# Optimization experiments

Measured on AMD Instinct MI355X. Metric: run time of the kernel, lower is better.

The kernel has to match this reference:

```python
import jax, jax.numpy as jnp
import numpy as np


def setup_inputs() -> dict:
    key = jax.random.key(0)
    z = jax.random.normal(key, (8, 4096, 1024), dtype=jnp.float32)
    return {"z": z}


def reference(z):
    d = z.shape[-1]
    # sort descending along last dim
    z_sorted = -jnp.sort(-z, axis=-1)
    z_cumsum = jnp.cumsum(z_sorted, axis=-1)
    k = jnp.arange(1, d + 1, dtype=z.dtype)  # [d]
    rhs = 1 + k * z_sorted
    is_gt = (rhs > z_cumsum).astype(z.dtype)
    # largest k satisfying the support condition
    k_z = jnp.max(is_gt * k, axis=-1, keepdims=True)  # [..., 1]
    idx = k_z.astype(jnp.int32) - 1
    z_cumsum_k = jnp.take_along_axis(z_cumsum, idx, axis=-1)
    tau = (z_cumsum_k - 1) / k_z
    p = jnp.clip(z - tau, 0.0, None)
    return p
```

## Files before the change

kernel.cpp:

```cpp
#include <hip/hip_runtime.h>


#define ROW_D 1024
#define NEG_PAD -3.0e38f

typedef float f4 __attribute__((ext_vector_type(4)));

template <int CTRL, int RMASK>
__device__ __forceinline__ float dpp_mv(float x) {
    return __builtin_bit_cast(float, __builtin_amdgcn_update_dpp(
        __builtin_bit_cast(int, x), __builtin_bit_cast(int, x),
        CTRL, RMASK, 0xf, false));
}
__device__ __forceinline__ float dpp_sum_to63(float x) {
    x += dpp_mv<0x111, 0xf>(x);
    x += dpp_mv<0x112, 0xf>(x);
    x += dpp_mv<0x114, 0xf>(x);
    x += dpp_mv<0x118, 0xf>(x);
    x += dpp_mv<0x142, 0xa>(x);
    x += dpp_mv<0x143, 0xc>(x);
    return x;
}
__device__ __forceinline__ float dpp_max_to63(float x) {
    x = fmaxf(x, dpp_mv<0x111, 0xf>(x));
    x = fmaxf(x, dpp_mv<0x112, 0xf>(x));
    x = fmaxf(x, dpp_mv<0x114, 0xf>(x));
    x = fmaxf(x, dpp_mv<0x118, 0xf>(x));
    x = fmaxf(x, dpp_mv<0x142, 0xa>(x));
    x = fmaxf(x, dpp_mv<0x143, 0xc>(x));
    return x;
}
__device__ __forceinline__ float bcast63(float x) {
    return __builtin_bit_cast(float,
        __builtin_amdgcn_readlane(__builtin_bit_cast(int, x), 63));
}

__global__ __launch_bounds__(256) void sparsemax_kernel(
    const float* __restrict__ z, float* __restrict__ out, int nrows) {
    const int lane = (int)(threadIdx.x & 63u);
    const int row  = (int)(blockIdx.x << 2) + (int)(threadIdx.x >> 6);
    if (row >= nrows) return;

    const f4* __restrict__ zin = reinterpret_cast<const f4*>(z + (size_t)row * ROW_D);
    f4* __restrict__ pout      = reinterpret_cast<f4*>(out + (size_t)row * ROW_D);

    f4 v[4];
#pragma unroll
    for (int j = 0; j < 4; ++j) v[j] = zin[lane + 64 * j];

    float mj[4];
#pragma unroll
    for (int j = 0; j < 4; ++j)
        mj[j] = fmaxf(fmaxf(v[j].x, v[j].y), fmaxf(v[j].z, v[j].w));
    float m = fmaxf(fmaxf(mj[0], mj[1]), fmaxf(mj[2], mj[3]));
    m = bcast63(dpp_max_to63(m));
    const float lo0 = m - 1.0f;

    float c0 = NEG_PAD, c1 = NEG_PAD, c2 = NEG_PAD;
    int cnt = 0;
#pragma unroll
    for (int j = 0; j < 4; ++j) {
        const float e[4] = {v[j].x, v[j].y, v[j].z, v[j].w};
#pragma unroll
        for (int c = 0; c < 4; ++c) {
            const bool g = e[c] > lo0;
            c2 = g ? c1 : c2;
            c1 = g ? c0 : c1;
            c0 = g ? e[c] : c0;
            cnt += g ? 1 : 0;
        }
    }

    float t = lo0;
    if (__ballot(cnt > 3) == 0ULL) {
#pragma unroll 1
        for (int it = 0; it < 16; ++it) {
            const float d0 = c0 - t, d1 = c1 - t, d2 = c2 - t;
            const float s = fmaxf(d0, 0.0f) + (fmaxf(d1, 0.0f) + fmaxf(d2, 0.0f));
            int n = __popcll(__ballot(d0 > 0.0f));
            n += __popcll(__ballot(d1 > 0.0f));
            n += __popcll(__ballot(d2 > 0.0f));
            const float S = bcast63(dpp_sum_to63(s));
            const float t2 = t + (S - 1.0f) / (float)n;
            if (t2 - t <= 1e-6f) { t = t2; break; }
            t = t2;
        }
    } else {
#pragma unroll 1
        for (int it = 0; it < 24; ++it) {
            float sj[4];
            int n = 0;
#pragma unroll
            for (int j = 0; j < 4; ++j) {
                const float d0 = v[j].x - t, d1 = v[j].y - t;
                const float d2 = v[j].z - t, d3 = v[j].w - t;
                sj[j] = (fmaxf(d0, 0.0f) + fmaxf(d1, 0.0f)) +
                        (fmaxf(d2, 0.0f) + fmaxf(d3, 0.0f));
                n += __popcll(__ballot(d0 > 0.0f));
                n += __popcll(__ballot(d1 > 0.0f));
                n += __popcll(__ballot(d2 > 0.0f));
                n += __popcll(__ballot(d3 > 0.0f));
            }
            const float S = bcast63(dpp_sum_to63((sj[0] + sj[1]) + (sj[2] + sj[3])));
            const float t2 = t + (S - 1.0f) / (float)n;
            if (t2 - t <= 1e-6f) { t = t2; break; }
            t = t2;
        }
    }

#pragma unroll
    for (int j = 0; j < 4; ++j) {
        f4 o;
        o.x = fmaxf(v[j].x - t, 0.0f);
        o.y = fmaxf(v[j].y - t, 0.0f);
        o.z = fmaxf(v[j].z - t, 0.0f);
        o.w = fmaxf(v[j].w - t, 0.0f);
        __builtin_nontemporal_store(o, pout + lane + 64 * j);
    }
}

extern "C" void kernel_launch(void* const* d_in, const int* in_sizes, int n_in,
                              void* d_out, int out_size, void* d_ws, size_t ws_size,
                              hipStream_t stream) {
    const float* z = (const float*)d_in[0];
    float* out = (float*)d_out;
    const int n = in_sizes[0];
    const int nrows = n / ROW_D;
    const int blocks = (nrows + 3) / 4;
    sparsemax_kernel<<<blocks, 256, 0, stream>>>(z, out, nrows);
}
```

Baseline: 229.4 us.

## Process four rows per wave with register double-buffered prefetch of next row

Each wavefront now handles several consecutive rows, loading the next row into registers while computing tau for the current one. This hides global-load latency behind the iterative threshold search and cuts the grid to a quarter of the blocks. In exchange it uses more registers, may lower occupancy, and leaves fewer blocks to spread across the CUs.

```diff
diff --git a/kernel.cpp b/kernel.cpp
--- a/kernel.cpp
+++ b/kernel.cpp
@@ -2,6 +2,7 @@
 
 
 #define ROW_D 1024
+#define RPW   4
 #define NEG_PAD -3.0e38f
 
 typedef float f4 __attribute__((ext_vector_type(4)));
@@ -35,19 +36,7 @@
         __builtin_amdgcn_readlane(__builtin_bit_cast(int, x), 63));
 }
 
-__global__ __launch_bounds__(256) void sparsemax_kernel(
-    const float* __restrict__ z, float* __restrict__ out, int nrows) {
-    const int lane = (int)(threadIdx.x & 63u);
-    const int row  = (int)(blockIdx.x << 2) + (int)(threadIdx.x >> 6);
-    if (row >= nrows) return;
-
-    const f4* __restrict__ zin = reinterpret_cast<const f4*>(z + (size_t)row * ROW_D);
-    f4* __restrict__ pout      = reinterpret_cast<f4*>(out + (size_t)row * ROW_D);
-
-    f4 v[4];
-#pragma unroll
-    for (int j = 0; j < 4; ++j) v[j] = zin[lane + 64 * j];
-
+__device__ __forceinline__ float row_tau(const f4* __restrict__ v) {
     float mj[4];
 #pragma unroll
     for (int j = 0; j < 4; ++j)
@@ -107,15 +96,48 @@
             t = t2;
         }
     }
+    return t;
+}
+
+__global__ __launch_bounds__(256) void sparsemax_kernel(
+    const float* __restrict__ z, float* __restrict__ out, int nrows) {
+    const int lane  = (int)(threadIdx.x & 63u);
+    const int wslot = (int)(threadIdx.x >> 6);
+    const int base  = ((int)(blockIdx.x << 2) + wslot) * RPW;
+    if (base >= nrows) return;
+
+    f4 nxt[4], cur[4];
+    {
+        const f4* zr = reinterpret_cast<const f4*>(z + (size_t)base * ROW_D);
+#pragma unroll
+        for (int j = 0; j < 4; ++j) nxt[j] = zr[lane + 64 * j];
+    }
 
 #pragma unroll
-    for (int j = 0; j < 4; ++j) {
-        f4 o;
-        o.x = fmaxf(v[j].x - t, 0.0f);
-        o.y = fmaxf(v[j].y - t, 0.0f);
-        o.z = fmaxf(v[j].z - t, 0.0f);
-        o.w = fmaxf(v[j].w - t, 0.0f);
-        __builtin_nontemporal_store(o, pout + lane + 64 * j);
+    for (int i = 0; i < RPW; ++i) {
+        const int row = (base + i < nrows) ? base + i : nrows - 1;
+#pragma unroll
+        for (int j = 0; j < 4; ++j) cur[j] = nxt[j];
+
+        if (i + 1 < RPW) {
+            const int nrow = (base + i + 1 < nrows) ? base + i + 1 : nrows - 1;
+            const f4* zn = reinterpret_cast<const f4*>(z + (size_t)nrow * ROW_D);
+#pragma unroll
+            for (int j = 0; j < 4; ++j) nxt[j] = zn[lane + 64 * j];
+        }
+
+        const float t = row_tau(cur);
+
+        f4* po = reinterpret_cast<f4*>(out + (size_t)row * ROW_D);
+#pragma unroll
+        for (int j = 0; j < 4; ++j) {
+            f4 o;
+            o.x = fmaxf(cur[j].x - t, 0.0f);
+            o.y = fmaxf(cur[j].y - t, 0.0f);
+            o.z = fmaxf(cur[j].z - t, 0.0f);
+            o.w = fmaxf(cur[j].w - t, 0.0f);
+            __builtin_nontemporal_store(o, po + lane + 64 * j);
+        }
     }
 }
 
@@ -126,6 +148,7 @@
     float* out = (float*)d_out;
     const int n = in_sizes[0];
     const int nrows = n / ROW_D;
-    const int blocks = (nrows + 3) / 4;
+    const int rows_per_block = 4 * RPW;
+    const int blocks = (nrows + rows_per_block - 1) / rows_per_block;
     sparsemax_kernel<<<blocks, 256, 0, stream>>>(z, out, nrows);
 }
```

New measurement: 237.0 us. 3.3% more time.

## Split sparsemax into separate tau-computation and apply kernels

Applied to the files above, without the earlier changes.

Splits the fused kernel into two launches. The first computes each row's threshold and writes it to workspace, and the second rereads the input and applies the clip. The intent is to let each stage have simpler register usage and access patterns. The cost is reading the 128MB input twice plus an extra kernel launch.

```diff
diff --git a/kernel.cpp b/kernel.cpp
--- a/kernel.cpp
+++ b/kernel.cpp
@@ -35,15 +35,13 @@
         __builtin_amdgcn_readlane(__builtin_bit_cast(int, x), 63));
 }
 
-__global__ __launch_bounds__(256) void sparsemax_kernel(
-    const float* __restrict__ z, float* __restrict__ out, int nrows) {
+__global__ __launch_bounds__(256) void tau_kernel(
+    const float* __restrict__ z, float* __restrict__ taus, int nrows) {
     const int lane = (int)(threadIdx.x & 63u);
     const int row  = (int)(blockIdx.x << 2) + (int)(threadIdx.x >> 6);
     if (row >= nrows) return;
 
     const f4* __restrict__ zin = reinterpret_cast<const f4*>(z + (size_t)row * ROW_D);
-    f4* __restrict__ pout      = reinterpret_cast<f4*>(out + (size_t)row * ROW_D);
-
     f4 v[4];
 #pragma unroll
     for (int j = 0; j < 4; ++j) v[j] = zin[lane + 64 * j];
@@ -107,15 +105,28 @@
             t = t2;
         }
     }
+    if (lane == 0) taus[row] = t;
+}
 
+__global__ __launch_bounds__(256) void apply_kernel(
+    const float* __restrict__ z, const float* __restrict__ taus,
+    float* __restrict__ out, int nrows) {
+    const int r0  = (int)(blockIdx.x << 2);
+    const int tid = (int)threadIdx.x;
 #pragma unroll
-    for (int j = 0; j < 4; ++j) {
+    for (int i = 0; i < 4; ++i) {
+        const int row = r0 + i;
+        if (row >= nrows) return;
+        const float t = taus[row];
+        const f4* __restrict__ zi = reinterpret_cast<const f4*>(z + (size_t)row * ROW_D);
+        f4* __restrict__ po       = reinterpret_cast<f4*>(out + (size_t)row * ROW_D);
+        const f4 x = zi[tid];
         f4 o;
-        o.x = fmaxf(v[j].x - t, 0.0f);
-        o.y = fmaxf(v[j].y - t, 0.0f);
-        o.z = fmaxf(v[j].z - t, 0.0f);
-        o.w = fmaxf(v[j].w - t, 0.0f);
-        __builtin_nontemporal_store(o, pout + lane + 64 * j);
+        o.x = fmaxf(x.x - t, 0.0f);
+        o.y = fmaxf(x.y - t, 0.0f);
+        o.z = fmaxf(x.z - t, 0.0f);
+        o.w = fmaxf(x.w - t, 0.0f);
+        __builtin_nontemporal_store(o, po + tid);
     }
 }
 
@@ -124,8 +135,13 @@
                               hipStream_t stream) {
     const float* z = (const float*)d_in[0];
     float* out = (float*)d_out;
+    float* taus = (float*)d_ws;
     const int n = in_sizes[0];
     const int nrows = n / ROW_D;
-    const int blocks = (nrows + 3) / 4;
-    sparsemax_kernel<<<blocks, 256, 0, stream>>>(z, out, nrows);
+
+    const int blocksA = (nrows + 3) / 4;
+    tau_kernel<<<blocksA, 256, 0, stream>>>(z, taus, nrows);
+
+    const int blocksB = (nrows + 3) / 4;
+    apply_kernel<<<blocksB, 256, 0, stream>>>(z, taus, out, nrows);
 }
```

New measurement: 237.3 us. 3.4% more time.
